# Optimization experiments

Measured on AMD Instinct MI355X. Metric: run time of the kernel, lower is better.

## Reference

```python
import jax, jax.numpy as jnp
import numpy as np

B, C, E = 2, 1024, 1024
H = 16            # n_heads as declared (used as per-group feature dim due to module's reshape)
HD = E // H       # 64 — the axis actually batched over in attention


def setup_inputs() -> dict:
    key = jax.random.key(0)
    ks = jax.random.split(key, 5)
    scale = 0.02
    return {
        "x": jax.random.normal(ks[0], (B, C, E), dtype=jnp.float32),
        "W_q": jax.random.normal(ks[1], (E, E), dtype=jnp.float32) * scale,
        "W_k": jax.random.normal(ks[2], (E, E), dtype=jnp.float32) * scale,
        "W_v": jax.random.normal(ks[3], (E, E), dtype=jnp.float32) * scale,
        "W_o": jax.random.normal(ks[4], (E, E), dtype=jnp.float32) * scale,
    }


def reference(x, W_q, W_k, W_v, W_o):
    # nn.Linear: y = x @ W.T  (bias=False)
    def proj_split(W):
        y = jnp.einsum('bce,de->bcd', x, W)              # [B,C,E]
        # view(B, C, HD, H).transpose(1,2) -> [B, HD, C, H]  (faithful to source layout)
        return y.reshape(B, C, HD, H).transpose(0, 2, 1, 3)

    Q = proj_split(W_q)
    K = proj_split(W_k)
    V = proj_split(W_v)

    scale = 1.0 / jnp.sqrt(jnp.asarray(H, dtype=x.dtype))  # sqrt of last dim (= n_heads here)
    scores = jnp.einsum('bdqh,bdkh->bdqk', Q, K) * scale    # [B, HD, C, C]
    weights = jax.nn.softmax(scores, axis=-1)
    out = jnp.einsum('bdqk,bdkh->bdqh', weights, V)         # [B, HD, C, H]
    out = out.transpose(0, 2, 1, 3).reshape(B, C, E)        # [B, C, E]
    out = jnp.einsum('bce,de->bcd', out, W_o)
    return out  # dropout p=0.0 / eval mode: identity
```

## Files before the change

kernel.cpp:

```cpp
#include <hip/hip_runtime.h>
#include <stdint.h>
#include <math.h>


typedef __bf16   bf16x8 __attribute__((ext_vector_type(8)));
typedef float    f32x4  __attribute__((ext_vector_type(4)));

__device__ __forceinline__ unsigned short f2bf(float f) {
    unsigned int u = __float_as_uint(f);
    u += 0x7FFFu + ((u >> 16) & 1u);
    return (unsigned short)(u >> 16);
}
__device__ __forceinline__ float bflo(unsigned int u) { return __uint_as_float(u << 16); }

__device__ __forceinline__ unsigned int pkbf(float lo, float hi) {
    const unsigned int ulo = __float_as_uint(lo) + 0x8000u;
    const unsigned int uhi = __float_as_uint(hi) + 0x8000u;
    return __builtin_amdgcn_perm(uhi, ulo, 0x07060302u);
}

__global__ __launch_bounds__(256) void cast_to_bf16(
    const float* __restrict__ x,
    const float* __restrict__ w0, const float* __restrict__ w1,
    const float* __restrict__ w2, const float* __restrict__ w3,
    unsigned short* __restrict__ xb,
    unsigned short* __restrict__ b0, unsigned short* __restrict__ b1,
    unsigned short* __restrict__ b2, unsigned short* __restrict__ b3)
{
    const int z = blockIdx.y;
    const float* src;
    unsigned short* dst;
    size_t off = 0;
    float sc = 1.f;
    if (z < 2)       { src = x;  dst = xb; off = (size_t)z << 20; }
    else if (z == 2) { src = w0; dst = b0; sc = 0.36067376022224085f; }
    else if (z == 3) { src = w1; dst = b1; }
    else if (z == 4) { src = w2; dst = b2; }
    else             { src = w3; dst = b3; }
    const size_t i = off + ((size_t)blockIdx.x * 256 + threadIdx.x) * 4;
    const float4 v = *(const float4*)(src + i);
    *(ushort4*)(dst + i) = make_ushort4(f2bf(v.x * sc), f2bf(v.y * sc),
                                        f2bf(v.z * sc), f2bf(v.w * sc));
}

#define CSTR 68

__global__ __launch_bounds__(256) void gemm_bt_mfma(
    const unsigned short* __restrict__ A,
    const unsigned short* __restrict__ B0, const unsigned short* __restrict__ B1,
    const unsigned short* __restrict__ B2,
    void* __restrict__ C0, void* __restrict__ C1, void* __restrict__ C2,
    int M, int N, int K, int bf16out)
{
    const unsigned short* Bm = (blockIdx.z == 0) ? B0 : (blockIdx.z == 1) ? B1 : B2;
    void* Cm                 = (blockIdx.z == 0) ? C0 : (blockIdx.z == 1) ? C1 : C2;

    __shared__ __align__(16) unsigned short smem[8704];
    unsigned short* As = smem;
    unsigned short* Bs = smem + 2048;

    const int t    = threadIdx.x;
    const int lane = t & 63;
    const int w    = t >> 6;
    const int m0   = blockIdx.y * 64;
    const int n0   = blockIdx.x * 128;
    const int wm   = (w & 1) * 32;
    const int wn   = (w >> 1) * 64;

    const int r0 = t >> 2;
    const int c0 = (t & 3) * 8;
    const unsigned short* Apa = A  + (size_t)(m0 + r0) * K + c0;
    const unsigned short* Bpa = Bm + (size_t)(n0 + r0) * K + c0;
    const unsigned short* Bpb = Bm + (size_t)(n0 + r0 + 64) * K + c0;

    f32x4 acc[2][4];
#pragma unroll
    for (int i = 0; i < 2; ++i)
#pragma unroll
        for (int j = 0; j < 4; ++j) acc[i][j] = (f32x4){0.f, 0.f, 0.f, 0.f};

    const int fm = lane & 15;
    const int kg = lane >> 4;

    uint4 ra0 = *(const uint4*)(Apa);
    uint4 rb0 = *(const uint4*)(Bpa);
    uint4 rb1 = *(const uint4*)(Bpb);

    for (int k0 = 0; k0 < K; k0 += 32) {
        if (k0) __syncthreads();
        *(uint4*)&As[8 * t]        = ra0;
        *(uint4*)&Bs[8 * t]        = rb0;
        *(uint4*)&Bs[8 * t + 2048] = rb1;
        __syncthreads();

        if (k0 + 32 < K) {
            ra0 = *(const uint4*)(Apa + k0 + 32);
            rb0 = *(const uint4*)(Bpa + k0 + 32);
            rb1 = *(const uint4*)(Bpb + k0 + 32);
        }

        bf16x8 af[2], bfr[4];
#pragma unroll
        for (int im = 0; im < 2; ++im)
            af[im] = *(const bf16x8*)&As[(wm + im * 16 + fm) * 32 + kg * 8];
#pragma unroll
        for (int in = 0; in < 4; ++in)
            bfr[in] = *(const bf16x8*)&Bs[(wn + in * 16 + fm) * 32 + kg * 8];
#pragma unroll
        for (int im = 0; im < 2; ++im)
#pragma unroll
            for (int in = 0; in < 4; ++in)
                acc[im][in] = __builtin_amdgcn_mfma_f32_16x16x32_bf16(
                    af[im], bfr[in], acc[im][in], 0, 0, 0);
    }

    if (bf16out) {
        __syncthreads();
        unsigned short* R = smem + w * 2176;
        unsigned short* cp = (unsigned short*)Cm;
#pragma unroll
        for (int im = 0; im < 2; ++im)
#pragma unroll
            for (int in = 0; in < 4; ++in)
#pragma unroll
                for (int r = 0; r < 4; ++r)
                    R[(im * 16 + kg * 4 + r) * CSTR + in * 16 + fm] =
                        f2bf(acc[im][in][r]);
#pragma unroll
        for (int j = 0; j < 4; ++j) {
            const int rr = j * 8 + (lane >> 3);
            const int cc = (lane & 7) * 8;
            const uint4 v = *(const uint4*)&R[rr * CSTR + cc];
            *(uint4*)(cp + (size_t)(m0 + wm + rr) * N + n0 + wn + cc) = v;
        }
    } else {
#pragma unroll
        for (int im = 0; im < 2; ++im) {
#pragma unroll
            for (int in = 0; in < 4; ++in) {
                const int row = m0 + wm + im * 16 + kg * 4;
                const int col = n0 + wn + in * 16 + fm;
                float* cp = (float*)Cm;
#pragma unroll
                for (int r = 0; r < 4; ++r)
                    cp[(size_t)(row + r) * N + col] = acc[im][in][r];
            }
        }
    }
}

#define KSTR2 40
#define VSTR2 72
#define PSTR  80

__global__ __launch_bounds__(256) void attn_mfma(
    const unsigned short* __restrict__ Qb, const unsigned short* __restrict__ Kb,
    const unsigned short* __restrict__ Vb, unsigned short* __restrict__ Ob)
{
    __shared__ __align__(16) unsigned short Ks[64 * KSTR2];
    __shared__ __align__(16) unsigned short VsT[16 * VSTR2];
    __shared__ __align__(16) unsigned short Ps[128 * PSTR];
    __shared__ __align__(16) float Lsh[128];

    const int t    = threadIdx.x;
    const int lane = t & 63;
    const int wq   = t >> 6;
    const int fm   = lane & 15;
    const int kg   = lane >> 4;
    const int bh   = blockIdx.y;
    const size_t base = ((size_t)(bh >> 6) * 1024) * 1024 + (size_t)(bh & 63) * 16;
    const int q0 = blockIdx.x * 128;

    if (t < 128) {
        const int row = t >> 1, seg = t & 1;
        *(uint4*)&Ks[row * KSTR2 + 16 + seg * 8] = make_uint4(0, 0, 0, 0);
    }

    union { uint4 u; bf16x8 h; } zz; zz.u = make_uint4(0, 0, 0, 0);
    bf16x8 aq[2];
#pragma unroll
    for (int m = 0; m < 2; ++m) {
        if (kg < 2)
            aq[m] = *(const bf16x8*)(Qb + base +
                     (size_t)(q0 + wq * 32 + m * 16 + fm) * 1024 + kg * 8);
        else
            aq[m] = zz.h;
    }

    f32x4 oacc[2];
    float lp[2];
#pragma unroll
    for (int m = 0; m < 2; ++m) {
        oacc[m] = (f32x4){0.f, 0.f, 0.f, 0.f};
        lp[m] = 0.f;
    }

    for (int kt = 0; kt < 1024; kt += 64) {
        __syncthreads();
        if (t < 128) {
            const int row = t >> 1, seg = t & 1;
            *(uint4*)&Ks[row * KSTR2 + seg * 8] =
                *(const uint4*)(Kb + base + (size_t)(kt + row) * 1024 + seg * 8);
        } else {
            const int idx = t - 128;
            const int key = idx >> 1, half = idx & 1;
            uint4 v = *(const uint4*)(Vb + base + (size_t)(kt + key) * 1024 + half * 8);
            const unsigned short* pv = (const unsigned short*)&v;
#pragma unroll
            for (int d = 0; d < 8; ++d)
                VsT[(half * 8 + d) * VSTR2 + key] = pv[d];
        }
        __syncthreads();

        bf16x8 bk[4];
#pragma unroll
        for (int kn = 0; kn < 4; ++kn)
            bk[kn] = *(const bf16x8*)&Ks[(kn * 16 + fm) * KSTR2 + kg * 8];

#pragma unroll
        for (int kn = 0; kn < 4; ++kn) {
            f32x4 sm[2];
#pragma unroll
            for (int m = 0; m < 2; ++m)
                sm[m] = __builtin_amdgcn_mfma_f32_16x16x32_bf16(
                    bk[kn], aq[m], (f32x4){0.f, 0.f, 0.f, 0.f}, 0, 0, 0);
#pragma unroll
            for (int m = 0; m < 2; ++m) {
                const float p0 = __builtin_amdgcn_exp2f(sm[m][0]);
                const float p1 = __builtin_amdgcn_exp2f(sm[m][1]);
                const float p2 = __builtin_amdgcn_exp2f(sm[m][2]);
                const float p3 = __builtin_amdgcn_exp2f(sm[m][3]);
                lp[m] += (p0 + p1) + (p2 + p3);
                *(uint2*)&Ps[(wq * 32 + m * 16 + fm) * PSTR + kn * 16 + kg * 4] =
                    make_uint2(pkbf(p0, p1), pkbf(p2, p3));
            }
        }

        bf16x8 bv0 = *(const bf16x8*)&VsT[fm * VSTR2 + kg * 8];
        bf16x8 bv1 = *(const bf16x8*)&VsT[fm * VSTR2 + 32 + kg * 8];
#pragma unroll
        for (int m = 0; m < 2; ++m) {
            const int prow = wq * 32 + m * 16 + fm;
            bf16x8 ap0 = *(const bf16x8*)&Ps[prow * PSTR + kg * 8];
            bf16x8 ap1 = *(const bf16x8*)&Ps[prow * PSTR + 32 + kg * 8];
            oacc[m] = __builtin_amdgcn_mfma_f32_16x16x32_bf16(ap0, bv0, oacc[m], 0, 0, 0);
            oacc[m] = __builtin_amdgcn_mfma_f32_16x16x32_bf16(ap1, bv1, oacc[m], 0, 0, 0);
        }
    }

#pragma unroll
    for (int m = 0; m < 2; ++m) {
        float v = lp[m];
        v += __shfl_xor(v, 16, 64);
        v += __shfl_xor(v, 32, 64);
        if (kg == 0) Lsh[wq * 32 + m * 16 + fm] = v;
    }

#pragma unroll
    for (int m = 0; m < 2; ++m) {
        const float4 lr = *(const float4*)&Lsh[wq * 32 + m * 16 + kg * 4];
        const int qrow = q0 + wq * 32 + m * 16 + kg * 4;
        Ob[base + (size_t)(qrow + 0) * 1024 + fm] = f2bf(oacc[m][0] / lr.x);
        Ob[base + (size_t)(qrow + 1) * 1024 + fm] = f2bf(oacc[m][1] / lr.y);
        Ob[base + (size_t)(qrow + 2) * 1024 + fm] = f2bf(oacc[m][2] / lr.z);
        Ob[base + (size_t)(qrow + 3) * 1024 + fm] = f2bf(oacc[m][3] / lr.w);
    }
}

extern "C" void kernel_launch(void* const* d_in, const int* in_sizes, int n_in,
                              void* d_out, int out_size, void* d_ws, size_t ws_size,
                              hipStream_t stream) {
    const float* x  = (const float*)d_in[0];
    const float* Wq = (const float*)d_in[1];
    const float* Wk = (const float*)d_in[2];
    const float* Wv = (const float*)d_in[3];
    const float* Wo = (const float*)d_in[4];
    float* out = (float*)d_out;

    const int M = 2048, N = 1024, Kd = 1024;
    const size_t MEG = 1048576;
    unsigned short* ws = (unsigned short*)d_ws;
    unsigned short* xb  = ws;
    unsigned short* Wqb = ws + 2 * MEG;
    unsigned short* Wkb = ws + 3 * MEG;
    unsigned short* Wvb = ws + 4 * MEG;
    unsigned short* Wob = ws + 5 * MEG;
    unsigned short* Qb  = ws + 6 * MEG;
    unsigned short* Kb  = ws + 8 * MEG;
    unsigned short* Vb  = ws + 10 * MEG;
    unsigned short* Ob  = ws + 12 * MEG;

    dim3 gc(1024, 6, 1);
    cast_to_bf16<<<gc, 256, 0, stream>>>(x, Wq, Wk, Wv, Wo, xb, Wqb, Wkb, Wvb, Wob);

    dim3 g1(N / 128, M / 64, 3);
    gemm_bt_mfma<<<g1, 256, 0, stream>>>(xb, Wqb, Wkb, Wvb, Qb, Kb, Vb, M, N, Kd, 1);

    dim3 g2(8, 128, 1);
    attn_mfma<<<g2, 256, 0, stream>>>(Qb, Kb, Vb, Ob);

    dim3 g3(N / 128, M / 64, 1);
    gemm_bt_mfma<<<g3, 256, 0, stream>>>(Ob, Wob, Wob, Wob, out, out, out, M, N, Kd, 0);
}
```

Measured before the change: 150.5 us.

## Write V transposed from projection GEMM and double query rows per attention block

The projection GEMM now stores V in a transposed [batch, feature, token] layout through an LDS-staged epilogue. This lets the attention kernel load V tiles with vector loads instead of scalar transposing stores into shared memory. The attention block also grows from 128 to 256 query rows, so each K/V tile is reused across twice as many queries, and the P stride is padded to 84. The cost is more registers and LDS per block and half as many attention blocks, which may reduce occupancy.

```diff
diff --git a/kernel.cpp b/kernel.cpp
--- a/kernel.cpp
+++ b/kernel.cpp
@@ -11,7 +11,6 @@
     u += 0x7FFFu + ((u >> 16) & 1u);
     return (unsigned short)(u >> 16);
 }
-__device__ __forceinline__ float bflo(unsigned int u) { return __uint_as_float(u << 16); }
 
 __device__ __forceinline__ unsigned int pkbf(float lo, float hi) {
     const unsigned int ulo = __float_as_uint(lo) + 0x8000u;
@@ -50,10 +49,11 @@
     const unsigned short* __restrict__ B0, const unsigned short* __restrict__ B1,
     const unsigned short* __restrict__ B2,
     void* __restrict__ C0, void* __restrict__ C1, void* __restrict__ C2,
-    int M, int N, int K, int bf16out)
+    int M, int N, int K, int vt_last)
 {
     const unsigned short* Bm = (blockIdx.z == 0) ? B0 : (blockIdx.z == 1) ? B1 : B2;
     void* Cm                 = (blockIdx.z == 0) ? C0 : (blockIdx.z == 1) ? C1 : C2;
+    const int mode = (vt_last < 0) ? 0 : ((blockIdx.z == 2 && vt_last) ? 2 : 1);
 
     __shared__ __align__(16) unsigned short smem[8704];
     unsigned short* As = smem;
@@ -114,7 +114,7 @@
                     af[im], bfr[in], acc[im][in], 0, 0, 0);
     }
 
-    if (bf16out) {
+    if (mode == 1) {
         __syncthreads();
         unsigned short* R = smem + w * 2176;
         unsigned short* cp = (unsigned short*)Cm;
@@ -133,6 +133,28 @@
             const uint4 v = *(const uint4*)&R[rr * CSTR + cc];
             *(uint4*)(cp + (size_t)(m0 + wm + rr) * N + n0 + wn + cc) = v;
         }
+    } else if (mode == 2) {
+        __syncthreads();
+        unsigned short* R = smem + w * 2176;
+        unsigned short* vp = (unsigned short*)Cm;
+#pragma unroll
+        for (int im = 0; im < 2; ++im)
+#pragma unroll
+            for (int in = 0; in < 4; ++in)
+#pragma unroll
+                for (int r = 0; r < 4; ++r)
+                    R[(in * 16 + fm) * 34 + im * 16 + kg * 4 + r] =
+                        f2bf(acc[im][in][r]);
+        const int bidx   = (m0 + wm) >> 10;
+        const int tok_in = (m0 + wm) & 1023;
+#pragma unroll
+        for (int p = 0; p < 4; ++p) {
+            const int row = p * 16 + (lane >> 2);
+            const int cc  = (lane & 3) * 8;
+            const uint4 v = *(const uint4*)&R[row * 34 + cc];
+            *(uint4*)(vp + ((size_t)bidx << 20) +
+                      (size_t)(n0 + wn + row) * 1024 + tok_in + cc) = v;
+        }
     } else {
 #pragma unroll
         for (int im = 0; im < 2; ++im) {
@@ -151,16 +173,16 @@
 
 #define KSTR2 40
 #define VSTR2 72
-#define PSTR  80
+#define PSTR  84
 
 __global__ __launch_bounds__(256) void attn_mfma(
     const unsigned short* __restrict__ Qb, const unsigned short* __restrict__ Kb,
-    const unsigned short* __restrict__ Vb, unsigned short* __restrict__ Ob)
+    const unsigned short* __restrict__ Vt, unsigned short* __restrict__ Ob)
 {
     __shared__ __align__(16) unsigned short Ks[64 * KSTR2];
     __shared__ __align__(16) unsigned short VsT[16 * VSTR2];
-    __shared__ __align__(16) unsigned short Ps[128 * PSTR];
-    __shared__ __align__(16) float Lsh[128];
+    __shared__ __align__(16) unsigned short Ps[256 * PSTR];
+    __shared__ __align__(16) float Lsh[256];
 
     const int t    = threadIdx.x;
     const int lane = t & 63;
@@ -168,29 +190,33 @@
     const int fm   = lane & 15;
     const int kg   = lane >> 4;
     const int bh   = blockIdx.y;
-    const size_t base = ((size_t)(bh >> 6) * 1024) * 1024 + (size_t)(bh & 63) * 16;
-    const int q0 = blockIdx.x * 128;
+    const size_t base   = ((size_t)(bh >> 6) * 1024) * 1024 + (size_t)(bh & 63) * 16;
+    const size_t vtbase = ((size_t)(bh >> 6) << 20) + (size_t)(bh & 63) * 16 * 1024;
+    const int q0 = blockIdx.x * 256;
 
     if (t < 128) {
         const int row = t >> 1, seg = t & 1;
         *(uint4*)&Ks[row * KSTR2 + 16 + seg * 8] = make_uint4(0, 0, 0, 0);
     }
 
+    const int krow = t >> 1,         kseg = t & 1;
+    const int vd   = (t - 128) >> 3, vc   = (t - 128) & 7;
+
     union { uint4 u; bf16x8 h; } zz; zz.u = make_uint4(0, 0, 0, 0);
-    bf16x8 aq[2];
-#pragma unroll
-    for (int m = 0; m < 2; ++m) {
+    bf16x8 aq[4];
+#pragma unroll
+    for (int m = 0; m < 4; ++m) {
         if (kg < 2)
             aq[m] = *(const bf16x8*)(Qb + base +
-                     (size_t)(q0 + wq * 32 + m * 16 + fm) * 1024 + kg * 8);
+                     (size_t)(q0 + wq * 64 + m * 16 + fm) * 1024 + kg * 8);
         else
             aq[m] = zz.h;
     }
 
-    f32x4 oacc[2];
-    float lp[2];
-#pragma unroll
-    for (int m = 0; m < 2; ++m) {
+    f32x4 oacc[4];
+    float lp[4];
+#pragma unroll
+    for (int m = 0; m < 4; ++m) {
         oacc[m] = (f32x4){0.f, 0.f, 0.f, 0.f};
         lp[m] = 0.f;
     }
@@ -198,17 +224,11 @@
     for (int kt = 0; kt < 1024; kt += 64) {
         __syncthreads();
         if (t < 128) {
-            const int row = t >> 1, seg = t & 1;
-            *(uint4*)&Ks[row * KSTR2 + seg * 8] =
-                *(const uint4*)(Kb + base + (size_t)(kt + row) * 1024 + seg * 8);
+            *(uint4*)&Ks[krow * KSTR2 + kseg * 8] =
+                *(const uint4*)(Kb + base + (size_t)(kt + krow) * 1024 + kseg * 8);
         } else {
-            const int idx = t - 128;
-            const int key = idx >> 1, half = idx & 1;
-            uint4 v = *(const uint4*)(Vb + base + (size_t)(kt + key) * 1024 + half * 8);
-            const unsigned short* pv = (const unsigned short*)&v;
-#pragma unroll
-            for (int d = 0; d < 8; ++d)
-                VsT[(half * 8 + d) * VSTR2 + key] = pv[d];
+            *(uint4*)&VsT[vd * VSTR2 + vc * 8] =
+                *(const uint4*)(Vt + vtbase + (size_t)vd * 1024 + kt + vc * 8);
         }
         __syncthreads();
 
@@ -219,19 +239,19 @@
 
 #pragma unroll
         for (int kn = 0; kn < 4; ++kn) {
-            f32x4 sm[2];
-#pragma unroll
-            for (int m = 0; m < 2; ++m)
+            f32x4 sm[4];
+#pragma unroll
+            for (int m = 0; m < 4; ++m)
                 sm[m] = __builtin_amdgcn_mfma_f32_16x16x32_bf16(
                     bk[kn], aq[m], (f32x4){0.f, 0.f, 0.f, 0.f}, 0, 0, 0);
 #pragma unroll
-            for (int m = 0; m < 2; ++m) {
+            for (int m = 0; m < 4; ++m) {
                 const float p0 = __builtin_amdgcn_exp2f(sm[m][0]);
                 const float p1 = __builtin_amdgcn_exp2f(sm[m][1]);
                 const float p2 = __builtin_amdgcn_exp2f(sm[m][2]);
                 const float p3 = __builtin_amdgcn_exp2f(sm[m][3]);
                 lp[m] += (p0 + p1) + (p2 + p3);
-                *(uint2*)&Ps[(wq * 32 + m * 16 + fm) * PSTR + kn * 16 + kg * 4] =
+                *(uint2*)&Ps[(wq * 64 + m * 16 + fm) * PSTR + kn * 16 + kg * 4] =
                     make_uint2(pkbf(p0, p1), pkbf(p2, p3));
             }
         }
@@ -239,8 +259,8 @@
         bf16x8 bv0 = *(const bf16x8*)&VsT[fm * VSTR2 + kg * 8];
         bf16x8 bv1 = *(const bf16x8*)&VsT[fm * VSTR2 + 32 + kg * 8];
 #pragma unroll
-        for (int m = 0; m < 2; ++m) {
-            const int prow = wq * 32 + m * 16 + fm;
+        for (int m = 0; m < 4; ++m) {
+            const int prow = wq * 64 + m * 16 + fm;
             bf16x8 ap0 = *(const bf16x8*)&Ps[prow * PSTR + kg * 8];
             bf16x8 ap1 = *(const bf16x8*)&Ps[prow * PSTR + 32 + kg * 8];
             oacc[m] = __builtin_amdgcn_mfma_f32_16x16x32_bf16(ap0, bv0, oacc[m], 0, 0, 0);
@@ -249,17 +269,17 @@
     }
 
 #pragma unroll
-    for (int m = 0; m < 2; ++m) {
+    for (int m = 0; m < 4; ++m) {
         float v = lp[m];
         v += __shfl_xor(v, 16, 64);
         v += __shfl_xor(v, 32, 64);
-        if (kg == 0) Lsh[wq * 32 + m * 16 + fm] = v;
-    }
-
-#pragma unroll
-    for (int m = 0; m < 2; ++m) {
-        const float4 lr = *(const float4*)&Lsh[wq * 32 + m * 16 + kg * 4];
-        const int qrow = q0 + wq * 32 + m * 16 + kg * 4;
+        if (kg == 0) Lsh[wq * 64 + m * 16 + fm] = v;
+    }
+
+#pragma unroll
+    for (int m = 0; m < 4; ++m) {
+        const float4 lr = *(const float4*)&Lsh[wq * 64 + m * 16 + kg * 4];
+        const int qrow = q0 + wq * 64 + m * 16 + kg * 4;
         Ob[base + (size_t)(qrow + 0) * 1024 + fm] = f2bf(oacc[m][0] / lr.x);
         Ob[base + (size_t)(qrow + 1) * 1024 + fm] = f2bf(oacc[m][1] / lr.y);
         Ob[base + (size_t)(qrow + 2) * 1024 + fm] = f2bf(oacc[m][2] / lr.z);
@@ -287,18 +307,18 @@
     unsigned short* Wob = ws + 5 * MEG;
     unsigned short* Qb  = ws + 6 * MEG;
     unsigned short* Kb  = ws + 8 * MEG;
-    unsigned short* Vb  = ws + 10 * MEG;
+    unsigned short* Vtb = ws + 10 * MEG;
     unsigned short* Ob  = ws + 12 * MEG;
 
     dim3 gc(1024, 6, 1);
     cast_to_bf16<<<gc, 256, 0, stream>>>(x, Wq, Wk, Wv, Wo, xb, Wqb, Wkb, Wvb, Wob);
 
     dim3 g1(N / 128, M / 64, 3);
-    gemm_bt_mfma<<<g1, 256, 0, stream>>>(xb, Wqb, Wkb, Wvb, Qb, Kb, Vb, M, N, Kd, 1);
-
-    dim3 g2(8, 128, 1);
-    attn_mfma<<<g2, 256, 0, stream>>>(Qb, Kb, Vb, Ob);
+    gemm_bt_mfma<<<g1, 256, 0, stream>>>(xb, Wqb, Wkb, Wvb, Qb, Kb, Vtb, M, N, Kd, 1);
+
+    dim3 g2(4, 128, 1);
+    attn_mfma<<<g2, 256, 0, stream>>>(Qb, Kb, Vtb, Ob);
 
     dim3 g3(N / 128, M / 64, 1);
-    gemm_bt_mfma<<<g3, 256, 0, stream>>>(Ob, Wob, Wob, Wob, out, out, out, M, N, Kd, 0);
-}
+    gemm_bt_mfma<<<g3, 256, 0, stream>>>(Ob, Wob, Wob, Wob, out, out, out, M, N, Kd, -1);
+}
```

Measured after the change: 152.1 us. No clear change (+1.1%).
